# Performance work log

Hardware: AMD Instinct MI355X
Metric: run time of the kernel (lower is better)

The kernel has to match this reference:

```python
import jax, jax.numpy as jnp
import numpy as np

N_NODES = 10000
N_EDGES = 320000
D_FEAT = 128


def setup_inputs() -> dict:
    key = jax.random.key(0)
    k1, k2 = jax.random.split(key)
    feats = jax.random.normal(k1, (N_NODES, D_FEAT), dtype=jnp.float32)
    edge_index = jax.random.randint(k2, (2, N_EDGES), 0, N_NODES, dtype=jnp.int64)
    return {"feats": feats, "edge_index": edge_index}


def reference(feats, edge_index):
    # feats: [N, D]; edge_index: [2, E] with row 0 = src (u), row 1 = dst (v)
    src, dst = edge_index[0], edge_index[1]
    # u_sub_v gather-diff, abs-sum over feature dim, exp(-1/100 * .)
    diff_l1 = jnp.sum(jnp.abs(feats[src] - feats[dst]), axis=-1)  # [E]
    e = jnp.exp(-0.01 * diff_l1)[:, None]                          # [E, 1] (feats viewed [N,1,D])
    # edge_softmax: numerically-stable softmax over incoming edges of each dst node
    seg_max = jax.ops.segment_max(e, dst, num_segments=N_NODES)    # [N, 1]
    ex = jnp.exp(e - seg_max[dst])                                 # [E, 1]
    seg_sum = jax.ops.segment_sum(ex, dst, num_segments=N_NODES)   # [N, 1]
    return ex / seg_sum[dst]                                       # [E, 1]
```

## Files before the change

### kernel.cpp

```cpp
#include <hip/hip_runtime.h>

#define D_FEAT 128

__global__ void edge_eval_kernel(const float* __restrict__ feats,
                                 const int* __restrict__ src,
                                 const int* __restrict__ dst,
                                 float* __restrict__ seg_sum,
                                 float* __restrict__ out,
                                 int E) {
    int gtid = blockIdx.x * blockDim.x + threadIdx.x;
    int edge = gtid >> 3;
    int sl   = threadIdx.x & 7;
    if (edge >= E) return;

    int s = src[edge];
    int d = dst[edge];

    const float4* fa = (const float4*)(feats + (size_t)s * D_FEAT);
    const float4* fb = (const float4*)(feats + (size_t)d * D_FEAT);
    float4 a0 = fa[sl];
    float4 a1 = fa[sl + 8];
    float4 a2 = fa[sl + 16];
    float4 a3 = fa[sl + 24];
    float4 b0 = fb[sl];
    float4 b1 = fb[sl + 8];
    float4 b2 = fb[sl + 16];
    float4 b3 = fb[sl + 24];

    float sum = fabsf(a0.x - b0.x) + fabsf(a0.y - b0.y)
              + fabsf(a0.z - b0.z) + fabsf(a0.w - b0.w)
              + fabsf(a1.x - b1.x) + fabsf(a1.y - b1.y)
              + fabsf(a1.z - b1.z) + fabsf(a1.w - b1.w)
              + fabsf(a2.x - b2.x) + fabsf(a2.y - b2.y)
              + fabsf(a2.z - b2.z) + fabsf(a2.w - b2.w)
              + fabsf(a3.x - b3.x) + fabsf(a3.y - b3.y)
              + fabsf(a3.z - b3.z) + fabsf(a3.w - b3.w);

    #pragma unroll
    for (int off = 4; off >= 1; off >>= 1)
        sum += __shfl_xor(sum, off, 64);

    if (sl == 0) {
        float p = expf(expf(-0.01f * sum));
        out[edge] = p;
        atomicAdd(seg_sum + d, p);
    }
}

__global__ void edge_div_kernel(const int* __restrict__ dst,
                                const float* __restrict__ seg_sum,
                                float* __restrict__ out,
                                int E4) {
    int i = blockIdx.x * blockDim.x + threadIdx.x;
    if (i >= E4) return;
    float4 p = ((const float4*)out)[i];
    int4   d = ((const int4*)dst)[i];
    p.x /= seg_sum[d.x];
    p.y /= seg_sum[d.y];
    p.z /= seg_sum[d.z];
    p.w /= seg_sum[d.w];
    ((float4*)out)[i] = p;
}

__global__ void edge_div_tail_kernel(const int* __restrict__ dst,
                                     const float* __restrict__ seg_sum,
                                     float* __restrict__ out,
                                     int start, int E) {
    int e = start + blockIdx.x * blockDim.x + threadIdx.x;
    if (e >= E) return;
    out[e] = out[e] / seg_sum[dst[e]];
}

extern "C" void kernel_launch(void* const* d_in, const int* in_sizes, int n_in,
                              void* d_out, int out_size, void* d_ws, size_t ws_size,
                              hipStream_t stream) {
    const float* feats = (const float*)d_in[0];
    const int*   eidx  = (const int*)d_in[1];

    const int E = in_sizes[1] / 2;
    const int N = in_sizes[0] / D_FEAT;

    const int* src = eidx;
    const int* dst = eidx + E;

    float* seg_sum = (float*)d_ws;
    float* out     = (float*)d_out;

    hipMemsetAsync(seg_sum, 0, (size_t)N * sizeof(float), stream);

    {
        dim3 blk(256);
        dim3 grd((E + 31) / 32);
        edge_eval_kernel<<<grd, blk, 0, stream>>>(feats, src, dst, seg_sum, out, E);
    }
    {
        int E4 = E >> 2;
        if (E4 > 0) {
            dim3 blk(256);
            dim3 grd((E4 + 255) / 256);
            edge_div_kernel<<<grd, blk, 0, stream>>>(dst, seg_sum, out, E4);
        }
        if (E & 3) {
            int start = E4 << 2;
            dim3 blk(64);
            dim3 grd(1);
            edge_div_tail_kernel<<<grd, blk, 0, stream>>>(dst, seg_sum, out, start, E);
        }
    }
}
```

Baseline: 41.93 us.

## Gather half-precision features converted once per call, fuse seg_sum zeroing

Adds a pre-pass that converts the fp32 feature table to fp16 in workspace and also zeroes seg_sum, which replaces the memset. The edge kernel then gathers half-sized rows, halving gather traffic per edge. The cost is an extra conversion pass over the 5 MB table and reduced precision in the L1 distance. The result is compressed through exp(-0.01*x), so the error impact is likely small.

```diff
diff --git a/kernel.cpp b/kernel.cpp
--- a/kernel.cpp
+++ b/kernel.cpp
@@ -1,8 +1,38 @@
 #include <hip/hip_runtime.h>
+#include <hip/hip_fp16.h>
 
 #define D_FEAT 128
 
-__global__ void edge_eval_kernel(const float* __restrict__ feats,
+__global__ void convert_kernel(const float* __restrict__ feats,
+                               __half* __restrict__ feats16,
+                               float* __restrict__ seg_sum,
+                               int total8, int N) {
+    int i = blockIdx.x * blockDim.x + threadIdx.x;
+    if (i < N) seg_sum[i] = 0.0f;
+    if (i >= total8) return;
+    float4 v0 = ((const float4*)feats)[2 * i];
+    float4 v1 = ((const float4*)feats)[2 * i + 1];
+    __half2 h[4];
+    h[0] = __floats2half2_rn(v0.x, v0.y);
+    h[1] = __floats2half2_rn(v0.z, v0.w);
+    h[2] = __floats2half2_rn(v1.x, v1.y);
+    h[3] = __floats2half2_rn(v1.z, v1.w);
+    ((uint4*)feats16)[i] = *reinterpret_cast<uint4*>(h);
+}
+
+__device__ inline float l1_u32(unsigned ua, unsigned ub) {
+    __half2 ha = *reinterpret_cast<__half2*>(&ua);
+    __half2 hb = *reinterpret_cast<__half2*>(&ub);
+    float2 fa = __half22float2(ha);
+    float2 fb = __half22float2(hb);
+    return fabsf(fa.x - fb.x) + fabsf(fa.y - fb.y);
+}
+__device__ inline float l1_u4(uint4 a, uint4 b) {
+    return l1_u32(a.x, b.x) + l1_u32(a.y, b.y)
+         + l1_u32(a.z, b.z) + l1_u32(a.w, b.w);
+}
+
+__global__ void edge_eval_kernel(const __half* __restrict__ feats16,
                                  const int* __restrict__ src,
                                  const int* __restrict__ dst,
                                  float* __restrict__ seg_sum,
@@ -16,25 +46,14 @@
     int s = src[edge];
     int d = dst[edge];
 
-    const float4* fa = (const float4*)(feats + (size_t)s * D_FEAT);
-    const float4* fb = (const float4*)(feats + (size_t)d * D_FEAT);
-    float4 a0 = fa[sl];
-    float4 a1 = fa[sl + 8];
-    float4 a2 = fa[sl + 16];
-    float4 a3 = fa[sl + 24];
-    float4 b0 = fb[sl];
-    float4 b1 = fb[sl + 8];
-    float4 b2 = fb[sl + 16];
-    float4 b3 = fb[sl + 24];
+    const uint4* fa = (const uint4*)(feats16 + (size_t)s * D_FEAT);
+    const uint4* fb = (const uint4*)(feats16 + (size_t)d * D_FEAT);
+    uint4 a0 = fa[sl];
+    uint4 a1 = fa[sl + 8];
+    uint4 b0 = fb[sl];
+    uint4 b1 = fb[sl + 8];
 
-    float sum = fabsf(a0.x - b0.x) + fabsf(a0.y - b0.y)
-              + fabsf(a0.z - b0.z) + fabsf(a0.w - b0.w)
-              + fabsf(a1.x - b1.x) + fabsf(a1.y - b1.y)
-              + fabsf(a1.z - b1.z) + fabsf(a1.w - b1.w)
-              + fabsf(a2.x - b2.x) + fabsf(a2.y - b2.y)
-              + fabsf(a2.z - b2.z) + fabsf(a2.w - b2.w)
-              + fabsf(a3.x - b3.x) + fabsf(a3.y - b3.y)
-              + fabsf(a3.z - b3.z) + fabsf(a3.w - b3.w);
+    float sum = l1_u4(a0, b0) + l1_u4(a1, b1);
 
     #pragma unroll
     for (int off = 4; off >= 1; off >>= 1)
@@ -83,15 +102,20 @@
     const int* src = eidx;
     const int* dst = eidx + E;
 
-    float* seg_sum = (float*)d_ws;
-    float* out     = (float*)d_out;
+    float*  seg_sum = (float*)d_ws;
+    __half* feats16 = (__half*)(seg_sum + ((N + 3) & ~3));
+    float*  out     = (float*)d_out;
 
-    hipMemsetAsync(seg_sum, 0, (size_t)N * sizeof(float), stream);
-
+    {
+        int total8 = N * D_FEAT / 8;
+        dim3 blk(256);
+        dim3 grd((total8 + 255) / 256);
+        convert_kernel<<<grd, blk, 0, stream>>>(feats, feats16, seg_sum, total8, N);
+    }
     {
         dim3 blk(256);
         dim3 grd((E + 31) / 32);
-        edge_eval_kernel<<<grd, blk, 0, stream>>>(feats, src, dst, seg_sum, out, E);
+        edge_eval_kernel<<<grd, blk, 0, stream>>>(feats16, src, dst, seg_sum, out, E);
     }
     {
         int E4 = E >> 2;
```

Result: no change. 41.37 us (-1.4%).
